# Optimization experiments

Hardware: AMD Instinct MI355X
Metric: run time of the kernel (lower is better)

The kernel has to match this reference:

```python
import jax, jax.numpy as jnp
import numpy as np

DIM = 2048
N_HEADS = 16
Q_LORA = 1536
KV_LORA = 512
NOPE = 128
ROPE = 64
QK_D = NOPE + ROPE  # 192
V_D = 128
EPS = 1e-6
B, S = 2, 2048


def rmsnorm(x, w, eps=EPS):
    return x * jax.lax.rsqrt(jnp.mean(x * x, axis=-1, keepdims=True) + eps) * w


def rotate_pe(x, cos, sin):
    # x: [B, S, H, ROPE]; cos/sin: [S, ROPE] -> broadcast [1, S, 1, ROPE]
    c = cos[None, :, None, :]
    s = sin[None, :, None, :]
    x1, x2 = jnp.split(x, 2, axis=-1)
    rot = jnp.concatenate([-x2, x1], axis=-1)
    return x * c + rot * s


def setup_inputs() -> dict:
    key = jax.random.key(0)
    ks = jax.random.split(key, 8)
    std = 0.02
    x = jax.random.normal(ks[0], (B, S, DIM), dtype=jnp.float32)
    # proper rotary tables
    inv_freq = 1.0 / (10000.0 ** (np.arange(0, ROPE, 2, dtype=np.float32) / ROPE))
    t = np.arange(S, dtype=np.float32)
    freqs = np.outer(t, inv_freq)  # [S, ROPE/2]
    emb = np.concatenate([freqs, freqs], axis=-1)  # [S, ROPE]
    cos = jnp.asarray(np.cos(emb))
    sin = jnp.asarray(np.sin(emb))
    wq_a = jax.random.normal(ks[1], (Q_LORA, DIM), dtype=jnp.float32) * std
    q_norm_w = jnp.ones((Q_LORA,), dtype=jnp.float32)
    wq_b = jax.random.normal(ks[2], (N_HEADS * QK_D, Q_LORA), dtype=jnp.float32) * std
    wkv_a = jax.random.normal(ks[3], (KV_LORA + ROPE, DIM), dtype=jnp.float32) * std
    kv_norm_w = jnp.ones((KV_LORA,), dtype=jnp.float32)
    wkv_b = jax.random.normal(ks[4], (N_HEADS * (NOPE + V_D), KV_LORA), dtype=jnp.float32) * std
    wo = jax.random.normal(ks[5], (DIM, N_HEADS * V_D), dtype=jnp.float32) * std
    return {"x": x, "cos": cos, "sin": sin, "wq_a": wq_a, "q_norm_w": q_norm_w,
            "wq_b": wq_b, "wkv_a": wkv_a, "kv_norm_w": kv_norm_w, "wkv_b": wkv_b, "wo": wo}


def mla_forward(x, cos, sin, wq_a, q_norm_w, wq_b, wkv_a, kv_norm_w, wkv_b, wo):
    bsz, seqlen, _ = x.shape
    scale = QK_D ** (-0.5)
    # Q path: low-rank down-proj -> RMSNorm -> up-proj
    q = rmsnorm(x @ wq_a.T, q_norm_w) @ wq_b.T
    q = q.reshape(bsz, seqlen, N_HEADS, QK_D)
    q_nope, q_pe = q[..., :NOPE], q[..., NOPE:]
    q_pe = rotate_pe(q_pe, cos, sin)
    q = jnp.concatenate([q_nope, q_pe], axis=-1)
    # KV path: shared low-rank latent + single rope slice
    kv = x @ wkv_a.T  # [B, S, KV_LORA + ROPE]
    kv_c, k_pe = kv[..., :KV_LORA], kv[..., KV_LORA:]
    k_pe = rotate_pe(k_pe[:, :, None, :], cos, sin)  # [B, S, 1, ROPE]
    kvb = rmsnorm(kv_c, kv_norm_w) @ wkv_b.T
    kvb = kvb.reshape(bsz, seqlen, N_HEADS, NOPE + V_D)
    k_nope, v = kvb[..., :NOPE], kvb[..., NOPE:]
    k = jnp.concatenate([k_nope, jnp.broadcast_to(k_pe, (bsz, seqlen, N_HEADS, ROPE))], axis=-1)
    # causal attention
    scores = jnp.einsum('bqhd,bkhd->bhqk', q, k) * scale
    mask = jnp.tril(jnp.ones((seqlen, seqlen), dtype=bool))
    scores = jnp.where(mask[None, None], scores, jnp.finfo(scores.dtype).min)
    p = jax.nn.softmax(scores, axis=-1)
    out = jnp.einsum('bhqk,bkhd->bqhd', p, v)
    out = out.reshape(bsz, seqlen, N_HEADS * V_D)
    return out @ wo.T


def reference(x, cos, sin, wq_a, q_norm_w, wq_b, wkv_a, kv_norm_w, wkv_b, wo):
    return mla_forward(x, cos, sin, wq_a, q_norm_w, wq_b, wkv_a, kv_norm_w, wkv_b, wo)
```

## Files before the change

### kernel.cpp

```cpp
#include <hip/hip_runtime.h>

typedef unsigned short u16;
typedef __attribute__((ext_vector_type(8))) short short8;
typedef __attribute__((ext_vector_type(4))) float floatx4;

__device__ __forceinline__ float bf2f(u16 u) {
  union { unsigned int i; float f; } v; v.i = ((unsigned int)u) << 16; return v.f;
}
__device__ __forceinline__ u16 f2bf(float f) {
  union { float f; unsigned int i; } v; v.f = f;
  unsigned int u = v.i;
  u += 0x7fffu + ((u >> 16) & 1u);
  return (u16)(u >> 16);
}

__device__ __forceinline__ void gld_lds16(const void* g, void* l) {
  __builtin_amdgcn_global_load_lds(
      (const __attribute__((address_space(1))) unsigned int*)g,
      (__attribute__((address_space(3))) unsigned int*)l, 16, 0, 0);
}

__global__ __launch_bounds__(256) void repack_all_k(
    const float* __restrict__ x, const float* __restrict__ wqa,
    const float* __restrict__ wkva, const float* __restrict__ wqb,
    const float* __restrict__ wkvb, const float* __restrict__ wo,
    u16* __restrict__ xb, u16* __restrict__ wcat, u16* __restrict__ wqbb,
    u16* __restrict__ wkbb, u16* __restrict__ wob) {
  long i = ((long)blockIdx.x * 256 + threadIdx.x) * 4;
  int region = blockIdx.y;
  const float* s = nullptr; u16* d = nullptr; long n = 0;
  switch (region) {
    case 0: s = x;    d = xb;   n = 4096L * 2048; break;
    case 1: s = nullptr; d = wcat; n = 2304L * 2048; break;
    case 2: s = wqb;  d = wqbb; n = 3072L * 1536; break;
    case 3: s = wkvb; d = wkbb; n = 4096L * 512;  break;
    case 4: s = wo;   d = wob;  n = 2048L * 2048; break;
  }
  if (i >= n) return;
  float4 v;
  if (region == 1) {
    long r = i >> 11, c = i & 2047;
    if (r < 1536)      v = *(const float4*)(wqa + r * 2048 + c);
    else if (r < 2112) v = *(const float4*)(wkva + (r - 1536) * 2048 + c);
    else               v = (float4){0.f, 0.f, 0.f, 0.f};
  } else {
    v = *(const float4*)(s + i);
  }
  d[i + 0] = f2bf(v.x); d[i + 1] = f2bf(v.y);
  d[i + 2] = f2bf(v.z); d[i + 3] = f2bf(v.w);
}

#define SBAR()   __builtin_amdgcn_s_barrier()
#define SCHED0() __builtin_amdgcn_sched_barrier(0)

#define GPHASE(LAc, LBc, QQ, STAGE_STMT, WAIT_STMT)                              \
  {                                                                              \
    short8 a00 = *(const short8*)&(LAc)[agbase + (2*(QQ)) * 1024 + g0];          \
    short8 a01 = *(const short8*)&(LAc)[agbase + (2*(QQ)) * 1024 + g1];          \
    short8 a10 = *(const short8*)&(LAc)[agbase + (2*(QQ)+1) * 1024 + g0];        \
    short8 a11 = *(const short8*)&(LAc)[agbase + (2*(QQ)+1) * 1024 + g1];        \
    if ((QQ) == 0) {                                                             \
      _Pragma("unroll")                                                          \
      for (int fj = 0; fj < 4; ++fj) {                                           \
        bfrg[fj][0] = *(const short8*)&(LBc)[bgbase + fj * 1024 + g0];           \
        bfrg[fj][1] = *(const short8*)&(LBc)[bgbase + fj * 1024 + g1];           \
      }                                                                          \
    }                                                                            \
    STAGE_STMT;                                                                  \
    WAIT_STMT;                                                                   \
    SCHED0();                                                                    \
    SBAR();                                                                      \
    asm volatile("s_waitcnt lgkmcnt(0)" ::: "memory");                           \
    SCHED0();                                                                    \
    __builtin_amdgcn_s_setprio(1);                                               \
    _Pragma("unroll")                                                            \
    for (int fj = 0; fj < 4; ++fj) {                                             \
      acc[2*(QQ)][fj]   = __builtin_amdgcn_mfma_f32_16x16x32_bf16(a00, bfrg[fj][0], acc[2*(QQ)][fj],   0, 0, 0); \
      acc[2*(QQ)][fj]   = __builtin_amdgcn_mfma_f32_16x16x32_bf16(a01, bfrg[fj][1], acc[2*(QQ)][fj],   0, 0, 0); \
      acc[2*(QQ)+1][fj] = __builtin_amdgcn_mfma_f32_16x16x32_bf16(a10, bfrg[fj][0], acc[2*(QQ)+1][fj], 0, 0, 0); \
      acc[2*(QQ)+1][fj] = __builtin_amdgcn_mfma_f32_16x16x32_bf16(a11, bfrg[fj][1], acc[2*(QQ)+1][fj], 0, 0, 0); \
    }                                                                            \
    __builtin_amdgcn_s_setprio(0);                                               \
    SCHED0();                                                                    \
    SBAR();                                                                      \
  }

template <int OUT_F32>
__device__ __forceinline__ void gemm256_tile(
    const u16* __restrict__ A, int lda, const u16* __restrict__ W, int ldw,
    void* __restrict__ Cv, int ldc, int K, int bm, int bn,
    u16* __restrict__ LA, u16* __restrict__ LB) {
  int tid = threadIdx.x;
  int lane = tid & 63, w = tid >> 6;
  int wr = w >> 2, wc = w & 3;
  int fr = lane & 15, fq = lane >> 4;

  int srow = lane >> 3;
  int sgl  = (lane & 7) ^ srow;

  int agbase = (wr * 128 + fr) * 64;
  int bgbase = (wc * 64 + fr) * 64;
  int g0 = ((0 * 4 + fq) ^ (fr & 7)) * 8;
  int g1 = ((1 * 4 + fq) ^ (fr & 7)) * 8;

  floatx4 acc[8][4];
#pragma unroll
  for (int i = 0; i < 8; i++)
#pragma unroll
    for (int j = 0; j < 4; j++) acc[i][j] = (floatx4){0.f, 0.f, 0.f, 0.f};

  auto stA = [&](int buf, int kt, int half) {
#pragma unroll
    for (int j = 0; j < 2; ++j) {
      int rbase = half * 128 + (w * 2 + j) * 8;
      gld_lds16(A + (size_t)(bm + rbase + srow) * lda + kt * 64 + sgl * 8,
                (void*)&LA[buf * 16384 + rbase * 64]);
    }
  };
  auto stB = [&](int buf, int kt, int half) {
#pragma unroll
    for (int j = 0; j < 2; ++j) {
      int rbase = half * 128 + (w * 2 + j) * 8;
      gld_lds16(W + (size_t)(bn + rbase + srow) * ldw + kt * 64 + sgl * 8,
                (void*)&LB[buf * 16384 + rbase * 64]);
    }
  };

  const u16* LA0 = LA;           const u16* LB0 = LB;
  const u16* LA1 = LA + 16384;   const u16* LB1 = LB + 16384;

  stB(0, 0, 0); stB(0, 0, 1);
  stA(0, 0, 0); stA(0, 0, 1);
  stB(1, 1, 0); stB(1, 1, 1);
  asm volatile("s_waitcnt vmcnt(4)" ::: "memory");
  SCHED0();
  SBAR();

  int NI = K >> 7;
  for (int i = 0; i < NI; ++i) {
    bool notlast = (i + 1 < NI);
    int t0 = 2 * i;
    {
      short8 bfrg[4][2];
      GPHASE(LA0, LB0, 0, stA(1, t0 + 1, 0), );
      GPHASE(LA0, LB0, 1, stA(1, t0 + 1, 1), );
      GPHASE(LA0, LB0, 2, if (notlast) stB(0, t0 + 2, 0), );
      GPHASE(LA0, LB0, 3, if (notlast) stB(0, t0 + 2, 1),
             if (notlast) { asm volatile("s_waitcnt vmcnt(4)" ::: "memory"); }
             else         { asm volatile("s_waitcnt vmcnt(0)" ::: "memory"); });
    }
    {
      short8 bfrg[4][2];
      GPHASE(LA1, LB1, 0, if (notlast) stA(0, t0 + 2, 0), );
      GPHASE(LA1, LB1, 1, if (notlast) stA(0, t0 + 2, 1), );
      GPHASE(LA1, LB1, 2, if (notlast) stB(1, t0 + 3, 0), );
      GPHASE(LA1, LB1, 3, if (notlast) stB(1, t0 + 3, 1),
             if (notlast) { asm volatile("s_waitcnt vmcnt(4)" ::: "memory"); });
    }
  }

  int cr = (lane >> 4) * 4, cc = lane & 15;
#pragma unroll
  for (int fi = 0; fi < 8; ++fi)
#pragma unroll
    for (int fj = 0; fj < 4; ++fj) {
      int col = bn + wc * 64 + fj * 16 + cc;
#pragma unroll
      for (int r = 0; r < 4; ++r) {
        size_t row = (size_t)(bm + wr * 128 + fi * 16 + cr + r);
        if (OUT_F32) ((float*)Cv)[row * ldc + col] = acc[fi][fj][r];
        else         ((u16*)Cv)[row * ldc + col] = f2bf(acc[fi][fj][r]);
      }
    }
}

template <int OUT_F32>
__global__ __launch_bounds__(512, 2) void gemm256_k(
    const u16* __restrict__ A, int lda,
    const u16* __restrict__ W, int ldw,
    void* __restrict__ Cv, int ldc, int K) {
  __shared__ __align__(16) u16 LAs[2][256 * 64];
  __shared__ __align__(16) u16 LBs[2][256 * 64];
  gemm256_tile<OUT_F32>(A, lda, W, ldw, Cv, ldc, K,
                        blockIdx.y * 256, blockIdx.x * 256, &LAs[0][0], &LBs[0][0]);
}

__global__ __launch_bounds__(512, 2) void gemm256_dual(
    const u16* __restrict__ A1, int lda1, const u16* __restrict__ W1, int ldw1,
    u16* __restrict__ C1, int ldc1, int K1, int nt1,
    const u16* __restrict__ A2, int lda2, const u16* __restrict__ W2, int ldw2,
    u16* __restrict__ C2, int ldc2, int K2) {
  __shared__ __align__(16) u16 LAs[2][256 * 64];
  __shared__ __align__(16) u16 LBs[2][256 * 64];
  int bx = blockIdx.x;
  if (bx < nt1)
    gemm256_tile<0>(A1, lda1, W1, ldw1, C1, ldc1, K1,
                    blockIdx.y * 256, bx * 256, &LAs[0][0], &LBs[0][0]);
  else
    gemm256_tile<0>(A2, lda2, W2, ldw2, C2, ldc2, K2,
                    blockIdx.y * 256, (bx - nt1) * 256, &LAs[0][0], &LBs[0][0]);
}

__global__ __launch_bounds__(256) void normrope_k(
    u16* __restrict__ qkv, const float* __restrict__ qnw,
    const float* __restrict__ kvnw, const float* __restrict__ cosb,
    const float* __restrict__ sinb, int S) {
  int row = blockIdx.x, tid = threadIdx.x;
  u16* p = qkv + (size_t)row * 2304;
  float s1 = 0.f, s2 = 0.f;
#pragma unroll
  for (int it = 0; it < 6; it++) { float v = bf2f(p[tid + 256 * it]); s1 += v * v; }
#pragma unroll
  for (int it = 0; it < 2; it++) { float v = bf2f(p[1536 + tid + 256 * it]); s2 += v * v; }
  for (int off = 32; off > 0; off >>= 1) {
    s1 += __shfl_down(s1, off);
    s2 += __shfl_down(s2, off);
  }
  __shared__ float red1[4], red2[4];
  if ((tid & 63) == 0) { red1[tid >> 6] = s1; red2[tid >> 6] = s2; }
  __syncthreads();
  float inv1 = rsqrtf((red1[0] + red1[1] + red1[2] + red1[3]) / 1536.f + 1e-6f);
  float inv2 = rsqrtf((red2[0] + red2[1] + red2[2] + red2[3]) / 512.f + 1e-6f);
#pragma unroll
  for (int it = 0; it < 6; it++) {
    int i = tid + 256 * it;
    p[i] = f2bf(bf2f(p[i]) * inv1 * qnw[i]);
  }
#pragma unroll
  for (int it = 0; it < 2; it++) {
    int i = tid + 256 * it;
    p[1536 + i] = f2bf(bf2f(p[1536 + i]) * inv2 * kvnw[i]);
  }
  if (tid < 32) {
    int pos = row % S;
    float c1 = cosb[pos * 64 + tid];
    float c2 = cosb[pos * 64 + tid + 32];
    float sn1 = sinb[pos * 64 + tid];
    float sn2 = sinb[pos * 64 + tid + 32];
    float x1 = bf2f(p[2048 + tid]), x2 = bf2f(p[2048 + tid + 32]);
    p[2048 + tid]      = f2bf(x1 * c1 - x2 * sn1);
    p[2048 + tid + 32] = f2bf(x2 * c2 + x1 * sn2);
  }
}

__global__ __launch_bounds__(256) void rope_k(
    u16* __restrict__ base, int row_stride, int head_stride, int head_off,
    const float* __restrict__ cosb, const float* __restrict__ sinb, int S) {
  int t = blockIdx.x;
  int h = blockIdx.y * 8 + (threadIdx.x >> 5);
  int i = threadIdx.x & 31;
  int pos = t % S;
  u16* p = base + (size_t)t * row_stride + h * head_stride + head_off;
  float c1 = cosb[pos * 64 + i];
  float c2 = cosb[pos * 64 + i + 32];
  float s1 = sinb[pos * 64 + i];
  float s2 = sinb[pos * 64 + i + 32];
  float x1 = bf2f(p[i]), x2 = bf2f(p[i + 32]);
  p[i]      = f2bf(x1 * c1 - x2 * s1);
  p[i + 32] = f2bf(x2 * c2 + x1 * s2);
}

__global__ __launch_bounds__(256) void vtrans_k(
    const u16* __restrict__ kvb, u16* __restrict__ vt, int S) {
  int tb = blockIdx.x, h = blockIdx.y, b = blockIdx.z;
  __shared__ __align__(16) u16 Ts[64][136];
  int tid = threadIdx.x;
#pragma unroll
  for (int it = 0; it < 4; it++) {
    int e = tid + 256 * it;
    int tok = e >> 4, c = e & 15;
    short8 v = *(const short8*)(kvb + (size_t)(b * S + tb * 64 + tok) * 4096 + h * 256 + 128 + c * 8);
    *(short8*)&Ts[tok][c * 8] = v;
  }
  __syncthreads();
  int vd = tid >> 1, half = (tid & 1) * 32;
  u16 tmp[32];
#pragma unroll
  for (int j = 0; j < 32; j++) tmp[j] = Ts[half + j][vd];
  u16* dst = vt + ((size_t)((b * 16 + h) * 128) + vd) * S + tb * 64 + half;
#pragma unroll
  for (int c = 0; c < 4; c++)
    *(short8*)(dst + c * 8) = *(short8*)&tmp[c * 8];
}

#define AT_BK 64
__global__ __launch_bounds__(256) void attn_mfma(
    const u16* __restrict__ qf, const u16* __restrict__ kvb,
    const u16* __restrict__ kpe, int kpe_stride, const u16* __restrict__ vt,
    u16* __restrict__ at, int S) {
  int id = blockIdx.x;
  int pair = id >> 5, hb = id & 31;
  int h = hb & 15, b = hb >> 4;
  int NT = S / AT_BK;
  int tid = threadIdx.x, lane = tid & 63, w = tid >> 6;
  int fr = lane & 15, fq = lane >> 4;
  int fs = fr & 7;

  __shared__ __align__(16) u16 Ksn[AT_BK * 128];
  __shared__ __align__(16) u16 Ksp[AT_BK * 64];
  __shared__ __align__(16) u16 Vts[128 * AT_BK];
  __shared__ __align__(16) u16 Ps[64 * AT_BK];

  const float scale = 0.07216878364870323f;

  for (int p = 0; p < 2; p++) {
    int qt = p ? (NT - 1 - pair) : pair;
    int q0 = qt * 64;

    short8 qfrag[6];
    {
      const u16* qrow = qf + (size_t)(b * S + q0 + w * 16 + fr) * 3072 + h * 192 + fq * 8;
#pragma unroll
      for (int ks = 0; ks < 6; ks++) qfrag[ks] = *(const short8*)(qrow + ks * 32);
    }

    floatx4 acc_o[8];
#pragma unroll
    for (int j = 0; j < 8; j++) acc_o[j] = (floatx4){0.f, 0.f, 0.f, 0.f};
    float m_r[4], l_r[4];
#pragma unroll
    for (int r = 0; r < 4; r++) { m_r[r] = -3e38f; l_r[r] = 0.f; }

    for (int kt = 0; kt <= qt; kt++) {
      int k0 = kt * AT_BK;
      size_t tokbase = (size_t)(b * S + k0);
#pragma unroll
      for (int c = 0; c < 4; c++) {
        int row = w * 16 + c * 4 + (lane >> 4);
        int cg = (lane & 15) ^ (row & 7);
        gld_lds16(kvb + (tokbase + row) * 4096 + h * 256 + cg * 8,
                  &Ksn[(w * 16 + c * 4) * 128]);
      }
#pragma unroll
      for (int c = 0; c < 2; c++) {
        int row = w * 16 + c * 8 + (lane >> 3);
        int cg = (lane & 7) ^ (row & 7);
        gld_lds16(kpe + (tokbase + row) * kpe_stride + cg * 8,
                  &Ksp[(w * 16 + c * 8) * 64]);
      }
#pragma unroll
      for (int c = 0; c < 4; c++) {
        int vd = w * 32 + c * 8 + (lane >> 3);
        int cg = (lane & 7) ^ (vd & 7);
        gld_lds16(vt + ((size_t)((b * 16 + h) * 128) + vd) * S + k0 + cg * 8,
                  &Vts[(w * 32 + c * 8) * 64]);
      }
      __syncthreads();

      floatx4 accs[4];
#pragma unroll
      for (int nt = 0; nt < 4; nt++) accs[nt] = (floatx4){0.f, 0.f, 0.f, 0.f};
      __builtin_amdgcn_s_setprio(1);
#pragma unroll
      for (int nt = 0; nt < 4; nt++) {
#pragma unroll
        for (int ks = 0; ks < 4; ks++) {
          short8 bf = *(const short8*)&Ksn[(nt * 16 + fr) * 128 + ((ks * 4 + fq) ^ fs) * 8];
          accs[nt] = __builtin_amdgcn_mfma_f32_16x16x32_bf16(qfrag[ks], bf, accs[nt], 0, 0, 0);
        }
#pragma unroll
        for (int ks = 0; ks < 2; ks++) {
          short8 bf = *(const short8*)&Ksp[(nt * 16 + fr) * 64 + ((ks * 4 + fq) ^ fs) * 8];
          accs[nt] = __builtin_amdgcn_mfma_f32_16x16x32_bf16(qfrag[4 + ks], bf, accs[nt], 0, 0, 0);
        }
      }
      __builtin_amdgcn_s_setprio(0);

      bool diag = (kt == qt);
#pragma unroll
      for (int nt = 0; nt < 4; nt++)
#pragma unroll
        for (int r = 0; r < 4; r++) {
          float s = accs[nt][r] * scale;
          if (diag) {
            int col = nt * 16 + fr;
            int row = fq * 4 + r;
            if (k0 + col > q0 + w * 16 + row) s = -3e38f;
          }
          accs[nt][r] = s;
        }

      float mx4[4];
      int grow = 0;
#pragma unroll
      for (int r = 0; r < 4; r++) {
        float mx = fmaxf(fmaxf(accs[0][r], accs[1][r]), fmaxf(accs[2][r], accs[3][r]));
        mx = fmaxf(mx, __shfl_xor(mx, 1));
        mx = fmaxf(mx, __shfl_xor(mx, 2));
        mx = fmaxf(mx, __shfl_xor(mx, 4));
        mx = fmaxf(mx, __shfl_xor(mx, 8));
        mx4[r] = mx;
        grow |= (mx > m_r[r] + 8.f) ? 1 : 0;
      }
      bool resc = __any(grow);
      float alpha[4];
      if (resc) {
#pragma unroll
        for (int r = 0; r < 4; r++) {
          float mnew = fmaxf(m_r[r], mx4[r]);
          alpha[r] = __expf(m_r[r] - mnew);
          m_r[r] = mnew;
          l_r[r] *= alpha[r];
        }
      }
#pragma unroll
      for (int nt = 0; nt < 4; nt++)
#pragma unroll
        for (int r = 0; r < 4; r++) {
          float pv = __expf(accs[nt][r] - m_r[r]);
          l_r[r] += pv;
          int row_p = w * 16 + fq * 4 + r;
          int col = nt * 16 + fr;
          Ps[row_p * 64 + (((col >> 3) ^ (row_p & 7)) * 8) + (col & 7)] = f2bf(pv);
        }
      __syncthreads();

      if (resc) {
#pragma unroll
        for (int j = 0; j < 8; j++)
#pragma unroll
          for (int r = 0; r < 4; r++) acc_o[j][r] *= alpha[r];
      }
      short8 pf0 = *(const short8*)&Ps[(w * 16 + fr) * 64 + (fq ^ fs) * 8];
      short8 pf1 = *(const short8*)&Ps[(w * 16 + fr) * 64 + ((4 + fq) ^ fs) * 8];
      __builtin_amdgcn_s_setprio(1);
#pragma unroll
      for (int j = 0; j < 8; j++) {
        short8 v0 = *(const short8*)&Vts[(j * 16 + fr) * 64 + (fq ^ fs) * 8];
        short8 v1 = *(const short8*)&Vts[(j * 16 + fr) * 64 + ((4 + fq) ^ fs) * 8];
        acc_o[j] = __builtin_amdgcn_mfma_f32_16x16x32_bf16(pf0, v0, acc_o[j], 0, 0, 0);
        acc_o[j] = __builtin_amdgcn_mfma_f32_16x16x32_bf16(pf1, v1, acc_o[j], 0, 0, 0);
      }
      __builtin_amdgcn_s_setprio(0);
      __syncthreads();
    }

    float inv_l[4];
#pragma unroll
    for (int r = 0; r < 4; r++) {
      float sm = l_r[r];
      sm += __shfl_xor(sm, 1);
      sm += __shfl_xor(sm, 2);
      sm += __shfl_xor(sm, 4);
      sm += __shfl_xor(sm, 8);
      inv_l[r] = 1.f / sm;
    }
#pragma unroll
    for (int j = 0; j < 8; j++)
#pragma unroll
      for (int r = 0; r < 4; r++) {
        size_t row = (size_t)(b * S + q0 + w * 16 + fq * 4 + r);
        at[row * 2048 + h * 128 + j * 16 + fr] = f2bf(acc_o[j][r] * inv_l[r]);
      }
  }
}

extern "C" void kernel_launch(void* const* d_in, const int* in_sizes, int n_in,
                              void* d_out, int out_size, void* d_ws, size_t ws_size,
                              hipStream_t stream) {
  (void)in_sizes; (void)n_in; (void)out_size; (void)ws_size;
  const float* x     = (const float*)d_in[0];
  const float* cosb  = (const float*)d_in[1];
  const float* sinb  = (const float*)d_in[2];
  const float* wq_a  = (const float*)d_in[3];
  const float* qnw   = (const float*)d_in[4];
  const float* wq_b  = (const float*)d_in[5];
  const float* wkv_a = (const float*)d_in[6];
  const float* kvnw  = (const float*)d_in[7];
  const float* wkv_b = (const float*)d_in[8];
  const float* wo    = (const float*)d_in[9];
  float* out = (float*)d_out;
  const int B = 2, S = 2048, T = B * S;

  char* wsb = (char*)d_ws;
  size_t off = 0;
  u16* xb   = (u16*)(wsb + off); off += (size_t)T * 2048 * 2;
  u16* wcat = (u16*)(wsb + off); off += (size_t)2304 * 2048 * 2;
  u16* wqbb = (u16*)(wsb + off); off += (size_t)3072 * 1536 * 2;
  u16* wkbb = (u16*)(wsb + off); off += (size_t)4096 * 512 * 2;
  u16* wob  = (u16*)(wsb + off); off += (size_t)2048 * 2048 * 2;
  u16* qkv  = (u16*)(wsb + off); off += (size_t)T * 2304 * 2;
  u16* qf   = (u16*)(wsb + off); off += (size_t)T * 3072 * 2;
  u16* kvb  = (u16*)(wsb + off); off += (size_t)T * 4096 * 2;
  u16* at   = (u16*)(wsb + off); off += (size_t)T * 2048 * 2;
  u16* vt   = xb;

  repack_all_k<<<dim3(8192, 5), 256, 0, stream>>>(
      x, wq_a, wkv_a, wq_b, wkv_b, wo, xb, wcat, wqbb, wkbb, wob);

  gemm256_k<0><<<dim3(2304 / 256, T / 256), 512, 0, stream>>>(xb, 2048, wcat, 2048, qkv, 2304, 2048);
  normrope_k<<<T, 256, 0, stream>>>(qkv, qnw, kvnw, cosb, sinb, S);
  gemm256_dual<<<dim3(3072 / 256 + 4096 / 256, T / 256), 512, 0, stream>>>(
      qkv, 2304, wqbb, 1536, qf, 3072, 1536, 3072 / 256,
      qkv + 1536, 2304, wkbb, 512, kvb, 4096, 512);
  rope_k<<<dim3(T, 2), 256, 0, stream>>>(qf, 3072, 192, 128, cosb, sinb, S);
  vtrans_k<<<dim3(S / 64, 16, B), 256, 0, stream>>>(kvb, vt, S);
  attn_mfma<<<dim3((S / 128) * 32), 256, 0, stream>>>(qf, kvb, qkv + 2048, 2304, vt, at, S);
  gemm256_k<1><<<dim3(2048 / 256, T / 256), 512, 0, stream>>>(at, 2048, wob, 2048, out, 2048, 2048);
}
```

Measured before the change: 464.0 us.

## Prefetch next K/V tile into registers during attention compute

The attention loop now loads the first K, K-rope and V^T tile before the loop starts. Inside the loop, each iteration issues global loads for the next tile into registers while the current tile's QK and PV MFMAs run. After a barrier it writes those registers into the swizzled LDS buffers, so load latency is hidden behind compute. It also drops the barrier between writing and reading P, since each wave only touches its own rows, and adds a launch bound asking for 2 blocks per CU. The risk is that the 10 staging registers per thread, combined with the occupancy bound, raise register pressure or cause spills.

```diff
diff --git a/kernel.cpp b/kernel.cpp
--- a/kernel.cpp
+++ b/kernel.cpp
@@ -284,7 +284,7 @@
 }
 
 #define AT_BK 64
-__global__ __launch_bounds__(256) void attn_mfma(
+__global__ __launch_bounds__(256, 2) void attn_mfma(
     const u16* __restrict__ qf, const u16* __restrict__ kvb,
     const u16* __restrict__ kpe, int kpe_stride, const u16* __restrict__ vt,
     u16* __restrict__ at, int S) {
@@ -302,6 +302,7 @@
   __shared__ __align__(16) u16 Ps[64 * AT_BK];
 
   const float scale = 0.07216878364870323f;
+  const size_t vbase = (size_t)((b * 16 + h) * 128);
 
   for (int p = 0; p < 2; p++) {
     int qt = p ? (NT - 1 - pair) : pair;
@@ -321,9 +322,8 @@
 #pragma unroll
     for (int r = 0; r < 4; r++) { m_r[r] = -3e38f; l_r[r] = 0.f; }
 
-    for (int kt = 0; kt <= qt; kt++) {
-      int k0 = kt * AT_BK;
-      size_t tokbase = (size_t)(b * S + k0);
+    {
+      size_t tokbase = (size_t)(b * S);
 #pragma unroll
       for (int c = 0; c < 4; c++) {
         int row = w * 16 + c * 4 + (lane >> 4);
@@ -342,10 +342,39 @@
       for (int c = 0; c < 4; c++) {
         int vd = w * 32 + c * 8 + (lane >> 3);
         int cg = (lane & 7) ^ (vd & 7);
-        gld_lds16(vt + ((size_t)((b * 16 + h) * 128) + vd) * S + k0 + cg * 8,
-                  &Vts[(w * 32 + c * 8) * 64]);
-      }
-      __syncthreads();
+        gld_lds16(vt + (vbase + vd) * S + cg * 8, &Vts[(w * 32 + c * 8) * 64]);
+      }
+    }
+    asm volatile("s_waitcnt vmcnt(0)" ::: "memory");
+    SCHED0();
+    SBAR();
+    SCHED0();
+
+    for (int kt = 0; kt <= qt; kt++) {
+      int k0 = kt * AT_BK;
+      bool pre = (kt < qt);
+
+      short8 stg[10];
+      if (pre) {
+        size_t tb1 = (size_t)(b * S + k0 + AT_BK);
+        int k1 = k0 + AT_BK;
+#pragma unroll
+        for (int c = 0; c < 4; c++) {
+          int row = w * 16 + c * 4 + (lane >> 4);
+          stg[c] = *(const short8*)(kvb + (tb1 + row) * 4096 + h * 256 + (lane & 15) * 8);
+        }
+#pragma unroll
+        for (int c = 0; c < 2; c++) {
+          int row = w * 16 + c * 8 + (lane >> 3);
+          stg[4 + c] = *(const short8*)(kpe + (tb1 + row) * kpe_stride + (lane & 7) * 8);
+        }
+#pragma unroll
+        for (int c = 0; c < 4; c++) {
+          int vd = w * 32 + c * 8 + (lane >> 3);
+          stg[6 + c] = *(const short8*)(vt + (vbase + vd) * S + k1 + (lane & 7) * 8);
+        }
+      }
+      SCHED0();
 
       floatx4 accs[4];
 #pragma unroll
@@ -413,7 +442,6 @@
           int col = nt * 16 + fr;
           Ps[row_p * 64 + (((col >> 3) ^ (row_p & 7)) * 8) + (col & 7)] = f2bf(pv);
         }
-      __syncthreads();
 
       if (resc) {
 #pragma unroll
@@ -432,7 +460,31 @@
         acc_o[j] = __builtin_amdgcn_mfma_f32_16x16x32_bf16(pf1, v1, acc_o[j], 0, 0, 0);
       }
       __builtin_amdgcn_s_setprio(0);
-      __syncthreads();
+
+      SCHED0();
+      SBAR();
+      SCHED0();
+      if (pre) {
+#pragma unroll
+        for (int c = 0; c < 4; c++) {
+          int row = w * 16 + c * 4 + (lane >> 4);
+          *(short8*)&Ksn[row * 128 + (((lane & 15) ^ (row & 7)) * 8)] = stg[c];
+        }
+#pragma unroll
+        for (int c = 0; c < 2; c++) {
+          int row = w * 16 + c * 8 + (lane >> 3);
+          *(short8*)&Ksp[row * 64 + (((lane & 7) ^ (row & 7)) * 8)] = stg[4 + c];
+        }
+#pragma unroll
+        for (int c = 0; c < 4; c++) {
+          int vd = w * 32 + c * 8 + (lane >> 3);
+          *(short8*)&Vts[vd * 64 + (((lane & 7) ^ (vd & 7)) * 8)] = stg[6 + c];
+        }
+        asm volatile("s_waitcnt lgkmcnt(0)" ::: "memory");
+        SCHED0();
+        SBAR();
+        SCHED0();
+      }
     }
 
     float inv_l[4];
```

Result: slower. 487.2 us (+5.0%).

## Use 128-tile GEMMs for projections, trim padding, and switch softmax to exp2

Applied to the files above, without the earlier changes.

Replaces the 256x256 double-buffered GEMM with a simpler single-buffered 128x128 MFMA tile for the QKV down-projection and the dual up-projection. The concatenated weight is padded only to 2176 rows instead of 2304, which cuts wasted work. Softmax now uses exp2f with the scale multiplied by log2(e), removing the implicit multiply inside exp. The simpler GEMM loses the software pipelining of the 256 kernel but gives more blocks to fill the CUs.

```diff
diff --git a/kernel.cpp b/kernel.cpp
--- a/kernel.cpp
+++ b/kernel.cpp
@@ -19,6 +19,9 @@
       (const __attribute__((address_space(1))) unsigned int*)g,
       (__attribute__((address_space(3))) unsigned int*)l, 16, 0, 0);
 }
+
+#define SBAR()   __builtin_amdgcn_s_barrier()
+#define SCHED0() __builtin_amdgcn_sched_barrier(0)
 
 __global__ __launch_bounds__(256) void repack_all_k(
     const float* __restrict__ x, const float* __restrict__ wqa,
@@ -31,7 +34,7 @@
   const float* s = nullptr; u16* d = nullptr; long n = 0;
   switch (region) {
     case 0: s = x;    d = xb;   n = 4096L * 2048; break;
-    case 1: s = nullptr; d = wcat; n = 2304L * 2048; break;
+    case 1: s = nullptr; d = wcat; n = 2176L * 2048; break;
     case 2: s = wqb;  d = wqbb; n = 3072L * 1536; break;
     case 3: s = wkvb; d = wkbb; n = 4096L * 512;  break;
     case 4: s = wo;   d = wob;  n = 2048L * 2048; break;
@@ -50,8 +53,87 @@
   d[i + 2] = f2bf(v.z); d[i + 3] = f2bf(v.w);
 }
 
-#define SBAR()   __builtin_amdgcn_s_barrier()
-#define SCHED0() __builtin_amdgcn_sched_barrier(0)
+template <int OUT_F32>
+__device__ __forceinline__ void gemm_tile(
+    const u16* __restrict__ A, int lda, const u16* __restrict__ W, int ldw,
+    void* __restrict__ Cv, int ldc, int K, int bm, int bn,
+    u16* Asm, u16* Bsm) {
+  int tid = threadIdx.x;
+  int lane = tid & 63, w = tid >> 6;
+  int wm = (w >> 1) * 64, wn = (w & 1) * 64;
+
+  floatx4 acc[4][4];
+#pragma unroll
+  for (int i = 0; i < 4; i++)
+#pragma unroll
+    for (int j = 0; j < 4; j++) acc[i][j] = (floatx4){0.f, 0.f, 0.f, 0.f};
+
+  int sr = lane >> 2;
+  int sc = (lane & 3) * 8;
+  int fr = lane & 15;
+  int fq = (lane >> 4) * 8;
+
+  for (int k0 = 0; k0 < K; k0 += 32) {
+#pragma unroll
+    for (int c = 0; c < 2; c++) {
+      int row = 32 * w + 16 * c + sr;
+      gld_lds16(A + (size_t)(bm + row) * lda + k0 + sc, &Asm[(32 * w + 16 * c) * 32]);
+      gld_lds16(W + (size_t)(bn + row) * ldw + k0 + sc, &Bsm[(32 * w + 16 * c) * 32]);
+    }
+    __syncthreads();
+    short8 af[4], bfr[4];
+#pragma unroll
+    for (int i = 0; i < 4; i++)
+      af[i] = *(const short8*)&Asm[(wm + i * 16 + fr) * 32 + fq];
+#pragma unroll
+    for (int j = 0; j < 4; j++)
+      bfr[j] = *(const short8*)&Bsm[(wn + j * 16 + fr) * 32 + fq];
+#pragma unroll
+    for (int i = 0; i < 4; i++)
+#pragma unroll
+      for (int j = 0; j < 4; j++)
+        acc[i][j] = __builtin_amdgcn_mfma_f32_16x16x32_bf16(af[i], bfr[j], acc[i][j], 0, 0, 0);
+    __syncthreads();
+  }
+
+  int cr = (lane >> 4) * 4, cc = lane & 15;
+#pragma unroll
+  for (int i = 0; i < 4; i++)
+#pragma unroll
+    for (int j = 0; j < 4; j++) {
+      int col = bn + wn + j * 16 + cc;
+#pragma unroll
+      for (int r = 0; r < 4; r++) {
+        size_t row = (size_t)(bm + wm + i * 16 + cr + r);
+        if (OUT_F32) ((float*)Cv)[row * ldc + col] = acc[i][j][r];
+        else         ((u16*)Cv)[row * ldc + col] = f2bf(acc[i][j][r]);
+      }
+    }
+}
+
+template <int OUT_F32>
+__global__ __launch_bounds__(256) void gemm_bt_mfma(
+    const u16* __restrict__ A, int lda,
+    const u16* __restrict__ W, int ldw,
+    void* __restrict__ Cv, int ldc, int K) {
+  __shared__ u16 Asm[128 * 32];
+  __shared__ u16 Bsm[128 * 32];
+  gemm_tile<OUT_F32>(A, lda, W, ldw, Cv, ldc, K, blockIdx.y * 128, blockIdx.x * 128, Asm, Bsm);
+}
+
+__global__ __launch_bounds__(256) void gemm_dual_mfma(
+    const u16* __restrict__ A1, int lda1, const u16* __restrict__ W1, int ldw1,
+    u16* __restrict__ C1, int ldc1, int K1, int nt1,
+    const u16* __restrict__ A2, int lda2, const u16* __restrict__ W2, int ldw2,
+    u16* __restrict__ C2, int ldc2, int K2) {
+  __shared__ u16 Asm[128 * 32];
+  __shared__ u16 Bsm[128 * 32];
+  int bx = blockIdx.x;
+  if (bx < nt1)
+    gemm_tile<0>(A1, lda1, W1, ldw1, C1, ldc1, K1, blockIdx.y * 128, bx * 128, Asm, Bsm);
+  else
+    gemm_tile<0>(A2, lda2, W2, ldw2, C2, ldc2, K2, blockIdx.y * 128, (bx - nt1) * 128, Asm, Bsm);
+}
 
 #define GPHASE(LAc, LBc, QQ, STAGE_STMT, WAIT_STMT)                              \
   {                                                                              \
@@ -185,28 +267,12 @@
                         blockIdx.y * 256, blockIdx.x * 256, &LAs[0][0], &LBs[0][0]);
 }
 
-__global__ __launch_bounds__(512, 2) void gemm256_dual(
-    const u16* __restrict__ A1, int lda1, const u16* __restrict__ W1, int ldw1,
-    u16* __restrict__ C1, int ldc1, int K1, int nt1,
-    const u16* __restrict__ A2, int lda2, const u16* __restrict__ W2, int ldw2,
-    u16* __restrict__ C2, int ldc2, int K2) {
-  __shared__ __align__(16) u16 LAs[2][256 * 64];
-  __shared__ __align__(16) u16 LBs[2][256 * 64];
-  int bx = blockIdx.x;
-  if (bx < nt1)
-    gemm256_tile<0>(A1, lda1, W1, ldw1, C1, ldc1, K1,
-                    blockIdx.y * 256, bx * 256, &LAs[0][0], &LBs[0][0]);
-  else
-    gemm256_tile<0>(A2, lda2, W2, ldw2, C2, ldc2, K2,
-                    blockIdx.y * 256, (bx - nt1) * 256, &LAs[0][0], &LBs[0][0]);
-}
-
 __global__ __launch_bounds__(256) void normrope_k(
     u16* __restrict__ qkv, const float* __restrict__ qnw,
     const float* __restrict__ kvnw, const float* __restrict__ cosb,
     const float* __restrict__ sinb, int S) {
   int row = blockIdx.x, tid = threadIdx.x;
-  u16* p = qkv + (size_t)row * 2304;
+  u16* p = qkv + (size_t)row * 2176;
   float s1 = 0.f, s2 = 0.f;
 #pragma unroll
   for (int it = 0; it < 6; it++) { float v = bf2f(p[tid + 256 * it]); s1 += v * v; }
@@ -301,7 +367,7 @@
   __shared__ __align__(16) u16 Vts[128 * AT_BK];
   __shared__ __align__(16) u16 Ps[64 * AT_BK];
 
-  const float scale = 0.07216878364870323f;
+  const float scale = 0.10411804518038971f;
 
   for (int p = 0; p < 2; p++) {
     int qt = p ? (NT - 1 - pair) : pair;
@@ -398,7 +464,7 @@
 #pragma unroll
         for (int r = 0; r < 4; r++) {
           float mnew = fmaxf(m_r[r], mx4[r]);
-          alpha[r] = __expf(m_r[r] - mnew);
+          alpha[r] = exp2f(m_r[r] - mnew);
           m_r[r] = mnew;
           l_r[r] *= alpha[r];
         }
@@ -407,7 +473,7 @@
       for (int nt = 0; nt < 4; nt++)
 #pragma unroll
         for (int r = 0; r < 4; r++) {
-          float pv = __expf(accs[nt][r] - m_r[r]);
+          float pv = exp2f(accs[nt][r] - m_r[r]);
           l_r[r] += pv;
           int row_p = w * 16 + fq * 4 + r;
           int col = nt * 16 + fr;
@@ -475,11 +541,11 @@
   char* wsb = (char*)d_ws;
   size_t off = 0;
   u16* xb   = (u16*)(wsb + off); off += (size_t)T * 2048 * 2;
-  u16* wcat = (u16*)(wsb + off); off += (size_t)2304 * 2048 * 2;
+  u16* wcat = (u16*)(wsb + off); off += (size_t)2176 * 2048 * 2;
   u16* wqbb = (u16*)(wsb + off); off += (size_t)3072 * 1536 * 2;
   u16* wkbb = (u16*)(wsb + off); off += (size_t)4096 * 512 * 2;
   u16* wob  = (u16*)(wsb + off); off += (size_t)2048 * 2048 * 2;
-  u16* qkv  = (u16*)(wsb + off); off += (size_t)T * 2304 * 2;
+  u16* qkv  = (u16*)(wsb + off); off += (size_t)T * 2176 * 2;
   u16* qf   = (u16*)(wsb + off); off += (size_t)T * 3072 * 2;
   u16* kvb  = (u16*)(wsb + off); off += (size_t)T * 4096 * 2;
   u16* at   = (u16*)(wsb + off); off += (size_t)T * 2048 * 2;
@@ -488,13 +554,13 @@
   repack_all_k<<<dim3(8192, 5), 256, 0, stream>>>(
       x, wq_a, wkv_a, wq_b, wkv_b, wo, xb, wcat, wqbb, wkbb, wob);
 
-  gemm256_k<0><<<dim3(2304 / 256, T / 256), 512, 0, stream>>>(xb, 2048, wcat, 2048, qkv, 2304, 2048);
+  gemm_bt_mfma<0><<<dim3(2176 / 128, T / 128), 256, 0, stream>>>(xb, 2048, wcat, 2048, qkv, 2176, 2048);
   normrope_k<<<T, 256, 0, stream>>>(qkv, qnw, kvnw, cosb, sinb, S);
-  gemm256_dual<<<dim3(3072 / 256 + 4096 / 256, T / 256), 512, 0, stream>>>(
-      qkv, 2304, wqbb, 1536, qf, 3072, 1536, 3072 / 256,
-      qkv + 1536, 2304, wkbb, 512, kvb, 4096, 512);
+  gemm_dual_mfma<<<dim3(3072 / 128 + 4096 / 128, T / 128), 256, 0, stream>>>(
+      qkv, 2176, wqbb, 1536, qf, 3072, 1536, 3072 / 128,
+      qkv + 1536, 2176, wkbb, 512, kvb, 4096, 512);
   rope_k<<<dim3(T, 2), 256, 0, stream>>>(qf, 3072, 192, 128, cosb, sinb, S);
   vtrans_k<<<dim3(S / 64, 16, B), 256, 0, stream>>>(kvb, vt, S);
-  attn_mfma<<<dim3((S / 128) * 32), 256, 0, stream>>>(qf, kvb, qkv + 2048, 2304, vt, at, S);
+  attn_mfma<<<dim3((S / 128) * 32), 256, 0, stream>>>(qf, kvb, qkv + 2048, 2176, vt, at, S);
   gemm256_k<1><<<dim3(2048 / 256, T / 256), 512, 0, stream>>>(at, 2048, wob, 2048, out, 2048, 2048);
 }
```

Result: slower. 480.4 us (+3.5%).
